# Kernel optimization log

Hardware: AMD Instinct MI355X
Metric: run time of the kernel (lower is better)

The kernel has to match this reference:

```python
import jax, jax.numpy as jnp
import numpy as np

N = 50000      # nodes
E = 800000     # edges (avg degree 16)
C = 5000       # clusters (Kongming compression)
D = 128        # in_features
OUT = 40       # out_features (classes)
K = 2          # propagation hops


def setup_inputs() -> dict:
    key = jax.random.key(0)
    k1, k2, k3, k4, k5, k6 = jax.random.split(key, 6)
    x = jax.random.normal(k1, (N, D), dtype=jnp.float32)
    edge_index = jax.random.randint(k2, (2, E), 0, N, dtype=jnp.int32)
    cluster_index = jax.random.randint(k3, (N,), 0, C, dtype=jnp.int32)
    rep_idx = jax.random.randint(k4, (C,), 0, N, dtype=jnp.int32)
    W = jax.random.normal(k5, (OUT, D), dtype=jnp.float32) / np.sqrt(D)
    b = jax.random.normal(k6, (OUT,), dtype=jnp.float32) * 0.01
    return {"x": x, "edge_index": edge_index, "cluster_index": cluster_index,
            "rep_idx": rep_idx, "W": W, "b": b}


def _gcn_propagate(x, edge_index, k_hops):
    # PUPropagate: K hops of D^{-1/2}(A+I)D^{-1/2} x (gcn_norm with self-loops)
    n = x.shape[0]
    loops = jnp.arange(n, dtype=edge_index.dtype)
    src = jnp.concatenate([edge_index[0], loops])
    dst = jnp.concatenate([edge_index[1], loops])
    deg = jax.ops.segment_sum(jnp.ones_like(src, dtype=x.dtype), dst, num_segments=n)
    dinv = jnp.where(deg > 0, jax.lax.rsqrt(deg), 0.0)
    norm = (dinv[src] * dinv[dst])[:, None]            # [E+N, 1]
    h = x
    for _ in range(k_hops):                            # small fixed hop count
        h = jax.ops.segment_sum(h[src] * norm, dst, num_segments=n)
    return h


def reference(x, edge_index, cluster_index, rep_idx, W, b):
    h = _gcn_propagate(x, edge_index, K)               # [N, D]
    # Kongming_Cluster: gather one representative row per cluster
    hc = h[rep_idx]                                    # [C, D]
    yc = hc @ W.T + b                                  # [C, OUT] dense linear on compressed rows
    # Kongming_Reconstruct: scatter back to all nodes by cluster index
    y = yc[cluster_index]                              # [N, OUT]
    return jax.nn.log_softmax(y, axis=1)
```

## Files before the change

### kernel.cpp

```cpp
#include <hip/hip_runtime.h>
#include <math.h>

#define N_NODES 50000
#define N_EDGES 800000
#define N_CLUST 5000
#define DIM     128
#define NOUT    40
#define SLOTS   64

#define FILL_PART   4
#define NODES_PER_P (N_NODES / FILL_PART)
#define FILL_CHUNKS 250
#define EI4         (N_EDGES / 4)
#define CI4         (EI4 / FILL_CHUNKS)

typedef __attribute__((ext_vector_type(8))) short short8;
typedef __attribute__((ext_vector_type(4))) float fvec4;
typedef __attribute__((ext_vector_type(4))) int ivec4;

__device__ __forceinline__ short bf16r(float v) {
    unsigned u = __float_as_uint(v);
    u = (u + 0x7FFFu + ((u >> 16) & 1u)) >> 16;
    return (short)u;
}
__device__ __forceinline__ unsigned pack_bf16x2(float a, float b) {
    unsigned ua = __float_as_uint(a);
    unsigned ub = __float_as_uint(b);
    ua = (ua + 0x7FFFu + ((ua >> 16) & 1u)) >> 16;
    ub = (ub + 0x7FFFu + ((ub >> 16) & 1u)) >> 16;
    return ua | (ub << 16);
}
__device__ __forceinline__ float2 unpack_bf16x2(unsigned v) {
    float2 r;
    r.x = __uint_as_float(v << 16);
    r.y = __uint_as_float(v & 0xFFFF0000u);
    return r;
}
__device__ __forceinline__ float4 unpack_bf16x4(uint2 v) {
    float4 r;
    r.x = __uint_as_float(v.x << 16);
    r.y = __uint_as_float(v.x & 0xFFFF0000u);
    r.z = __uint_as_float(v.y << 16);
    r.w = __uint_as_float(v.y & 0xFFFF0000u);
    return r;
}

__global__ __launch_bounds__(256) void fill_slots(const ivec4* __restrict__ src4,
                                                  const ivec4* __restrict__ dst4,
                                                  int* __restrict__ cnt,
                                                  unsigned short* __restrict__ slot) {
    int p = blockIdx.x & (FILL_PART - 1);
    int chunk = blockIdx.x >> 2;
    int lo = p * NODES_PER_P;
    int hi = lo + NODES_PER_P;
    int q0 = chunk * CI4;
    for (int i = threadIdx.x; i < CI4; i += 256) {
        ivec4 d4 = __builtin_nontemporal_load(&dst4[q0 + i]);
        ivec4 s4 = __builtin_nontemporal_load(&src4[q0 + i]);
        if (d4.x >= lo && d4.x < hi) {
            int pos = atomicAdd(&cnt[d4.x], 1);
            if (pos < SLOTS) slot[d4.x * SLOTS + pos] = (unsigned short)s4.x;
        }
        if (d4.y >= lo && d4.y < hi) {
            int pos = atomicAdd(&cnt[d4.y], 1);
            if (pos < SLOTS) slot[d4.y * SLOTS + pos] = (unsigned short)s4.y;
        }
        if (d4.z >= lo && d4.z < hi) {
            int pos = atomicAdd(&cnt[d4.z], 1);
            if (pos < SLOTS) slot[d4.z * SLOTS + pos] = (unsigned short)s4.z;
        }
        if (d4.w >= lo && d4.w < hi) {
            int pos = atomicAdd(&cnt[d4.w], 1);
            if (pos < SLOTS) slot[d4.w * SLOTS + pos] = (unsigned short)s4.w;
        }
    }
}

__global__ __launch_bounds__(256) void zgemm(const float* __restrict__ x,
                                             const float* __restrict__ W,
                                             const int* __restrict__ cnt,
                                             unsigned short* __restrict__ zs) {
    int lane = threadIdx.x & 63;
    int wv = threadIdx.x >> 6;
    int q = lane >> 4, r16 = lane & 15;
    int tile = blockIdx.x * 4 + wv;
    if (tile >= N_NODES / 16) return;

    short8 bfr[3][4];
    #pragma unroll
    for (int t = 0; t < 3; t++) {
        int o = t * 16 + r16;
        #pragma unroll
        for (int s = 0; s < 4; s++) {
            short8 f = {0, 0, 0, 0, 0, 0, 0, 0};
            if (o < NOUT) {
                const float* wp = W + o * DIM + s * 32 + q * 8;
                float4 w0 = *(const float4*)wp;
                float4 w1 = *(const float4*)(wp + 4);
                f[0] = bf16r(w0.x); f[1] = bf16r(w0.y);
                f[2] = bf16r(w0.z); f[3] = bf16r(w0.w);
                f[4] = bf16r(w1.x); f[5] = bf16r(w1.y);
                f[6] = bf16r(w1.z); f[7] = bf16r(w1.w);
            }
            bfr[t][s] = f;
        }
    }

    int node = tile * 16 + r16;
    float dn = rsqrtf((float)cnt[node] + 1.0f);
    short8 af[4];
    #pragma unroll
    for (int s = 0; s < 4; s++) {
        const float* xp = x + (size_t)node * DIM + s * 32 + q * 8;
        float4 a0 = *(const float4*)xp;
        float4 a1 = *(const float4*)(xp + 4);
        short8 f;
        f[0] = bf16r(dn * a0.x); f[1] = bf16r(dn * a0.y);
        f[2] = bf16r(dn * a0.z); f[3] = bf16r(dn * a0.w);
        f[4] = bf16r(dn * a1.x); f[5] = bf16r(dn * a1.y);
        f[6] = bf16r(dn * a1.z); f[7] = bf16r(dn * a1.w);
        af[s] = f;
    }

    fvec4 acc0 = {0, 0, 0, 0}, acc1 = {0, 0, 0, 0}, acc2 = {0, 0, 0, 0};
    #pragma unroll
    for (int s = 0; s < 4; s++) {
        acc0 = __builtin_amdgcn_mfma_f32_16x16x32_bf16(af[s], bfr[0][s], acc0, 0, 0, 0);
        acc1 = __builtin_amdgcn_mfma_f32_16x16x32_bf16(af[s], bfr[1][s], acc1, 0, 0, 0);
        acc2 = __builtin_amdgcn_mfma_f32_16x16x32_bf16(af[s], bfr[2][s], acc2, 0, 0, 0);
    }

    #pragma unroll
    for (int r = 0; r < 4; r++) {
        int nd = tile * 16 + q * 4 + r;
        unsigned short* zrow = zs + (size_t)nd * NOUT;
        zrow[r16]      = (unsigned short)bf16r(acc0[r]);
        zrow[16 + r16] = (unsigned short)bf16r(acc1[r]);
        if (r16 < 8) zrow[32 + r16] = (unsigned short)bf16r(acc2[r]);
    }
}

__global__ __launch_bounds__(256) void hop_all(const uint2* __restrict__ zs2,
                                               uint2* __restrict__ v12,
                                               const unsigned short* __restrict__ slot,
                                               const int* __restrict__ cnt) {
    int lane = threadIdx.x & 63;
    int g = lane / 10;
    int k = lane - g * 10;
    int wv = threadIdx.x >> 6;
    int n = blockIdx.x * 24 + wv * 6 + g;
    if (g >= 6 || n >= N_NODES) return;
    int c = cnt[n];
    int m = (c < SLOTS) ? c : SLOTS;
    float s = 1.0f / (float)(c + 1);
    float4 accA = unpack_bf16x4(zs2[n * 10 + k]);
    float4 accB; accB.x = accB.y = accB.z = accB.w = 0.0f;
    int base = n * SLOTS;
    int j = 0;
    for (; j + 7 < m; j += 8) {
        unsigned ss0 = *(const unsigned*)&slot[base + j];
        unsigned ss1 = *(const unsigned*)&slot[base + j + 2];
        unsigned ss2 = *(const unsigned*)&slot[base + j + 4];
        unsigned ss3 = *(const unsigned*)&slot[base + j + 6];
        float4 f0 = unpack_bf16x4(zs2[(int)(ss0 & 0xFFFFu) * 10 + k]);
        float4 f1 = unpack_bf16x4(zs2[(int)(ss0 >> 16) * 10 + k]);
        float4 f2 = unpack_bf16x4(zs2[(int)(ss1 & 0xFFFFu) * 10 + k]);
        float4 f3 = unpack_bf16x4(zs2[(int)(ss1 >> 16) * 10 + k]);
        float4 f4 = unpack_bf16x4(zs2[(int)(ss2 & 0xFFFFu) * 10 + k]);
        float4 f5 = unpack_bf16x4(zs2[(int)(ss2 >> 16) * 10 + k]);
        float4 f6 = unpack_bf16x4(zs2[(int)(ss3 & 0xFFFFu) * 10 + k]);
        float4 f7 = unpack_bf16x4(zs2[(int)(ss3 >> 16) * 10 + k]);
        accA.x += (f0.x + f1.x) + (f4.x + f5.x);
        accA.y += (f0.y + f1.y) + (f4.y + f5.y);
        accA.z += (f0.z + f1.z) + (f4.z + f5.z);
        accA.w += (f0.w + f1.w) + (f4.w + f5.w);
        accB.x += (f2.x + f3.x) + (f6.x + f7.x);
        accB.y += (f2.y + f3.y) + (f6.y + f7.y);
        accB.z += (f2.z + f3.z) + (f6.z + f7.z);
        accB.w += (f2.w + f3.w) + (f6.w + f7.w);
    }
    for (; j + 1 < m; j += 2) {
        unsigned ss0 = *(const unsigned*)&slot[base + j];
        float4 f0 = unpack_bf16x4(zs2[(int)(ss0 & 0xFFFFu) * 10 + k]);
        float4 f1 = unpack_bf16x4(zs2[(int)(ss0 >> 16) * 10 + k]);
        accA.x += f0.x + f1.x;  accA.y += f0.y + f1.y;
        accA.z += f0.z + f1.z;  accA.w += f0.w + f1.w;
    }
    if (j < m) {
        float4 f0 = unpack_bf16x4(zs2[(int)slot[base + j] * 10 + k]);
        accB.x += f0.x; accB.y += f0.y; accB.z += f0.z; accB.w += f0.w;
    }
    uint2 p;
    p.x = pack_bf16x2(s * (accA.x + accB.x), s * (accA.y + accB.y));
    p.y = pack_bf16x2(s * (accA.z + accB.z), s * (accA.w + accB.w));
    v12[n * 10 + k] = p;
}

__global__ __launch_bounds__(256) void rep_lsm(const unsigned* __restrict__ v1,
                                               const unsigned short* __restrict__ slot,
                                               const int* __restrict__ cnt,
                                               const int* __restrict__ rep_idx,
                                               const float2* __restrict__ b2,
                                               float2* __restrict__ yc2) {
    int lane = threadIdx.x & 63;
    int wv = threadIdx.x >> 6;
    int c = blockIdx.x * 4 + wv;
    if (c >= N_CLUST) return;
    int n = rep_idx[c];
    int cn = cnt[n];
    int m = (cn < SLOTS) ? cn : SLOTS;
    float dn = rsqrtf((float)(cn + 1));
    int g = lane / 20;
    int k = lane - g * 20;
    float2 acc; acc.x = 0.0f; acc.y = 0.0f;
    if (g == 0) acc = unpack_bf16x2(v1[n * 20 + k]);
    if (g < 3) {
        int base = n * SLOTS;
        for (int j = g; j < m; j += 3) {
            float2 f = unpack_bf16x2(v1[(int)slot[base + j] * 20 + k]);
            acc.x += f.x; acc.y += f.y;
        }
    }
    float t1x = __shfl(acc.x, lane + 20), t1y = __shfl(acc.y, lane + 20);
    float t2x = __shfl(acc.x, lane + 40), t2y = __shfl(acc.y, lane + 40);
    bool act = (lane < 20);
    float2 h; h.x = 0.0f; h.y = 0.0f;
    if (act) {
        float2 bb = b2[k];
        h.x = dn * (acc.x + t1x + t2x) + bb.x;
        h.y = dn * (acc.y + t1y + t2y) + bb.y;
    }
    float mx = act ? fmaxf(h.x, h.y) : -INFINITY;
    #pragma unroll
    for (int off = 32; off; off >>= 1) mx = fmaxf(mx, __shfl_xor(mx, off));
    float e = act ? (expf(h.x - mx) + expf(h.y - mx)) : 0.0f;
    #pragma unroll
    for (int off = 32; off; off >>= 1) e += __shfl_xor(e, off);
    float lg = mx + logf(e);
    if (act) {
        float2 o; o.x = h.x - lg; o.y = h.y - lg;
        yc2[(size_t)c * 20 + k] = o;
    }
}

__global__ void gather_out(const float4* __restrict__ yc4, const int* __restrict__ cidx,
                           float4* __restrict__ out4) {
    int t = blockIdx.x * blockDim.x + threadIdx.x;
    if (t >= N_NODES * (NOUT / 4)) return;
    int n = t / (NOUT / 4);
    int q = t - n * (NOUT / 4);
    out4[t] = yc4[(size_t)cidx[n] * (NOUT / 4) + q];
}

extern "C" void kernel_launch(void* const* d_in, const int* in_sizes, int n_in,
                              void* d_out, int out_size, void* d_ws, size_t ws_size,
                              hipStream_t stream) {
    const float* x    = (const float*)d_in[0];
    const int*   esrc = (const int*)d_in[1];
    const int*   edst = ((const int*)d_in[1]) + N_EDGES;
    const int*   cidx = (const int*)d_in[2];
    const int*   ridx = (const int*)d_in[3];
    const float* W    = (const float*)d_in[4];
    const float* b    = (const float*)d_in[5];
    float* out = (float*)d_out;

    char* ws = (char*)d_ws;
    size_t off = 0;
    auto alloc = [&](size_t bytes) { char* p = ws + off; off += (bytes + 255) & ~size_t(255); return p; };
    int*            cnt  = (int*)alloc(N_NODES * 4);
    unsigned short* slot = (unsigned short*)alloc((size_t)N_NODES * SLOTS * 2);
    unsigned short* zs   = (unsigned short*)alloc((size_t)N_NODES * NOUT * 2);
    unsigned*       v1   = (unsigned*)alloc((size_t)N_NODES * (NOUT / 2) * 4);
    float*          yc   = (float*)alloc((size_t)N_CLUST * NOUT * 4);
    (void)ws_size; (void)in_sizes; (void)n_in; (void)out_size;

    hipMemsetAsync(cnt, 0, N_NODES * 4, stream);

    const int B = 256;
    fill_slots<<<FILL_PART * FILL_CHUNKS, 256, 0, stream>>>((const ivec4*)esrc,
                                                            (const ivec4*)edst,
                                                            cnt, slot);
    zgemm<<<(N_NODES / 16 + 3) / 4, 256, 0, stream>>>(x, W, cnt, zs);
    hop_all<<<(N_NODES + 23) / 24, 256, 0, stream>>>((const uint2*)zs, (uint2*)v1,
                                                     slot, cnt);
    rep_lsm<<<(N_CLUST + 3) / 4, 256, 0, stream>>>((const unsigned*)v1, slot, cnt, ridx,
                                                   (const float2*)b, (float2*)yc);
    int gt = N_NODES * (NOUT / 4);
    gather_out<<<(gt + B - 1) / B, B, 0, stream>>>((const float4*)yc, cidx, (float4*)out);
}
```

Baseline: 162.3 us.

## Fuse slot fill, GEMM and cluster inversion; scatter log-softmax rows directly

The edge slot fill, the node GEMM and a new cluster-inverse build now run as disjoint block ranges of one launch, so the GEMM no longer waits for degrees. To make that possible, the degree normalisation moves out of the GEMM into the first hop, which now reads the degree of every neighbour. The cluster representative kernel writes its log-softmax row straight to every member node through the inverse lists, which drops the yc buffer and the gather kernel. In exchange the first hop does extra random degree reads, and clusters with more than 64 members would be silently truncated.

```diff
diff --git a/kernel.cpp b/kernel.cpp
--- a/kernel.cpp
+++ b/kernel.cpp
@@ -7,12 +7,18 @@
 #define DIM     128
 #define NOUT    40
 #define SLOTS   64
+#define CSLOT   64
 
 #define FILL_PART   4
 #define NODES_PER_P (N_NODES / FILL_PART)
 #define FILL_CHUNKS 250
 #define EI4         (N_EDGES / 4)
 #define CI4         (EI4 / FILL_CHUNKS)
+
+#define FILLB  1000
+#define ZB     782
+#define INVB   50
+#define GRID_A (FILLB + ZB + INVB)
 
 typedef __attribute__((ext_vector_type(8))) short short8;
 typedef __attribute__((ext_vector_type(4))) float fvec4;
@@ -45,98 +51,111 @@
     return r;
 }
 
-__global__ __launch_bounds__(256) void fill_slots(const ivec4* __restrict__ src4,
-                                                  const ivec4* __restrict__ dst4,
-                                                  int* __restrict__ cnt,
-                                                  unsigned short* __restrict__ slot) {
-    int p = blockIdx.x & (FILL_PART - 1);
-    int chunk = blockIdx.x >> 2;
-    int lo = p * NODES_PER_P;
-    int hi = lo + NODES_PER_P;
-    int q0 = chunk * CI4;
-    for (int i = threadIdx.x; i < CI4; i += 256) {
-        ivec4 d4 = __builtin_nontemporal_load(&dst4[q0 + i]);
-        ivec4 s4 = __builtin_nontemporal_load(&src4[q0 + i]);
-        if (d4.x >= lo && d4.x < hi) {
-            int pos = atomicAdd(&cnt[d4.x], 1);
-            if (pos < SLOTS) slot[d4.x * SLOTS + pos] = (unsigned short)s4.x;
-        }
-        if (d4.y >= lo && d4.y < hi) {
-            int pos = atomicAdd(&cnt[d4.y], 1);
-            if (pos < SLOTS) slot[d4.y * SLOTS + pos] = (unsigned short)s4.y;
-        }
-        if (d4.z >= lo && d4.z < hi) {
-            int pos = atomicAdd(&cnt[d4.z], 1);
-            if (pos < SLOTS) slot[d4.z * SLOTS + pos] = (unsigned short)s4.z;
-        }
-        if (d4.w >= lo && d4.w < hi) {
-            int pos = atomicAdd(&cnt[d4.w], 1);
-            if (pos < SLOTS) slot[d4.w * SLOTS + pos] = (unsigned short)s4.w;
-        }
-    }
-}
-
-__global__ __launch_bounds__(256) void zgemm(const float* __restrict__ x,
-                                             const float* __restrict__ W,
-                                             const int* __restrict__ cnt,
-                                             unsigned short* __restrict__ zs) {
+__global__ __launch_bounds__(256) void fused_A(const float* __restrict__ x,
+                                               const int* __restrict__ esrc,
+                                               const int* __restrict__ edst,
+                                               const int* __restrict__ cidx,
+                                               const float* __restrict__ W,
+                                               int* __restrict__ cnt,
+                                               int* __restrict__ ccnt,
+                                               unsigned short* __restrict__ slot,
+                                               unsigned short* __restrict__ zs,
+                                               unsigned short* __restrict__ cinv) {
     int lane = threadIdx.x & 63;
     int wv = threadIdx.x >> 6;
-    int q = lane >> 4, r16 = lane & 15;
-    int tile = blockIdx.x * 4 + wv;
-    if (tile >= N_NODES / 16) return;
-
-    short8 bfr[3][4];
-    #pragma unroll
-    for (int t = 0; t < 3; t++) {
-        int o = t * 16 + r16;
+
+    if (blockIdx.x < FILLB) {
+        const ivec4* src4 = (const ivec4*)esrc;
+        const ivec4* dst4 = (const ivec4*)edst;
+        int p = blockIdx.x & (FILL_PART - 1);
+        int chunk = blockIdx.x >> 2;
+        int lo = p * NODES_PER_P;
+        int hi = lo + NODES_PER_P;
+        int q0 = chunk * CI4;
+        for (int i = threadIdx.x; i < CI4; i += 256) {
+            ivec4 d4 = __builtin_nontemporal_load(&dst4[q0 + i]);
+            ivec4 s4 = __builtin_nontemporal_load(&src4[q0 + i]);
+            if (d4.x >= lo && d4.x < hi) {
+                int pos = atomicAdd(&cnt[d4.x], 1);
+                if (pos < SLOTS) slot[d4.x * SLOTS + pos] = (unsigned short)s4.x;
+            }
+            if (d4.y >= lo && d4.y < hi) {
+                int pos = atomicAdd(&cnt[d4.y], 1);
+                if (pos < SLOTS) slot[d4.y * SLOTS + pos] = (unsigned short)s4.y;
+            }
+            if (d4.z >= lo && d4.z < hi) {
+                int pos = atomicAdd(&cnt[d4.z], 1);
+                if (pos < SLOTS) slot[d4.z * SLOTS + pos] = (unsigned short)s4.z;
+            }
+            if (d4.w >= lo && d4.w < hi) {
+                int pos = atomicAdd(&cnt[d4.w], 1);
+                if (pos < SLOTS) slot[d4.w * SLOTS + pos] = (unsigned short)s4.w;
+            }
+        }
+    } else if (blockIdx.x < FILLB + ZB) {
+        int tile = (blockIdx.x - FILLB) * 4 + wv;
+        if (tile >= N_NODES / 16) return;
+        int q = lane >> 4, r16 = lane & 15;
+
+        short8 bfr[3][4];
+        #pragma unroll
+        for (int t = 0; t < 3; t++) {
+            int o = t * 16 + r16;
+            #pragma unroll
+            for (int s = 0; s < 4; s++) {
+                short8 f = {0, 0, 0, 0, 0, 0, 0, 0};
+                if (o < NOUT) {
+                    const float* wp = W + o * DIM + s * 32 + q * 8;
+                    float4 w0 = *(const float4*)wp;
+                    float4 w1 = *(const float4*)(wp + 4);
+                    f[0] = bf16r(w0.x); f[1] = bf16r(w0.y);
+                    f[2] = bf16r(w0.z); f[3] = bf16r(w0.w);
+                    f[4] = bf16r(w1.x); f[5] = bf16r(w1.y);
+                    f[6] = bf16r(w1.z); f[7] = bf16r(w1.w);
+                }
+                bfr[t][s] = f;
+            }
+        }
+
+        int node = tile * 16 + r16;
+        short8 af[4];
         #pragma unroll
         for (int s = 0; s < 4; s++) {
-            short8 f = {0, 0, 0, 0, 0, 0, 0, 0};
-            if (o < NOUT) {
-                const float* wp = W + o * DIM + s * 32 + q * 8;
-                float4 w0 = *(const float4*)wp;
-                float4 w1 = *(const float4*)(wp + 4);
-                f[0] = bf16r(w0.x); f[1] = bf16r(w0.y);
-                f[2] = bf16r(w0.z); f[3] = bf16r(w0.w);
-                f[4] = bf16r(w1.x); f[5] = bf16r(w1.y);
-                f[6] = bf16r(w1.z); f[7] = bf16r(w1.w);
-            }
-            bfr[t][s] = f;
-        }
-    }
-
-    int node = tile * 16 + r16;
-    float dn = rsqrtf((float)cnt[node] + 1.0f);
-    short8 af[4];
-    #pragma unroll
-    for (int s = 0; s < 4; s++) {
-        const float* xp = x + (size_t)node * DIM + s * 32 + q * 8;
-        float4 a0 = *(const float4*)xp;
-        float4 a1 = *(const float4*)(xp + 4);
-        short8 f;
-        f[0] = bf16r(dn * a0.x); f[1] = bf16r(dn * a0.y);
-        f[2] = bf16r(dn * a0.z); f[3] = bf16r(dn * a0.w);
-        f[4] = bf16r(dn * a1.x); f[5] = bf16r(dn * a1.y);
-        f[6] = bf16r(dn * a1.z); f[7] = bf16r(dn * a1.w);
-        af[s] = f;
-    }
-
-    fvec4 acc0 = {0, 0, 0, 0}, acc1 = {0, 0, 0, 0}, acc2 = {0, 0, 0, 0};
-    #pragma unroll
-    for (int s = 0; s < 4; s++) {
-        acc0 = __builtin_amdgcn_mfma_f32_16x16x32_bf16(af[s], bfr[0][s], acc0, 0, 0, 0);
-        acc1 = __builtin_amdgcn_mfma_f32_16x16x32_bf16(af[s], bfr[1][s], acc1, 0, 0, 0);
-        acc2 = __builtin_amdgcn_mfma_f32_16x16x32_bf16(af[s], bfr[2][s], acc2, 0, 0, 0);
-    }
-
-    #pragma unroll
-    for (int r = 0; r < 4; r++) {
-        int nd = tile * 16 + q * 4 + r;
-        unsigned short* zrow = zs + (size_t)nd * NOUT;
-        zrow[r16]      = (unsigned short)bf16r(acc0[r]);
-        zrow[16 + r16] = (unsigned short)bf16r(acc1[r]);
-        if (r16 < 8) zrow[32 + r16] = (unsigned short)bf16r(acc2[r]);
+            const fvec4* xp = (const fvec4*)(x + (size_t)node * DIM + s * 32 + q * 8);
+            fvec4 a0 = __builtin_nontemporal_load(xp);
+            fvec4 a1 = __builtin_nontemporal_load(xp + 1);
+            short8 f;
+            f[0] = bf16r(a0.x); f[1] = bf16r(a0.y);
+            f[2] = bf16r(a0.z); f[3] = bf16r(a0.w);
+            f[4] = bf16r(a1.x); f[5] = bf16r(a1.y);
+            f[6] = bf16r(a1.z); f[7] = bf16r(a1.w);
+            af[s] = f;
+        }
+
+        fvec4 acc0 = {0, 0, 0, 0}, acc1 = {0, 0, 0, 0}, acc2 = {0, 0, 0, 0};
+        #pragma unroll
+        for (int s = 0; s < 4; s++) {
+            acc0 = __builtin_amdgcn_mfma_f32_16x16x32_bf16(af[s], bfr[0][s], acc0, 0, 0, 0);
+            acc1 = __builtin_amdgcn_mfma_f32_16x16x32_bf16(af[s], bfr[1][s], acc1, 0, 0, 0);
+            acc2 = __builtin_amdgcn_mfma_f32_16x16x32_bf16(af[s], bfr[2][s], acc2, 0, 0, 0);
+        }
+
+        #pragma unroll
+        for (int r = 0; r < 4; r++) {
+            int nd = tile * 16 + q * 4 + r;
+            unsigned short* zrow = zs + (size_t)nd * NOUT;
+            __builtin_nontemporal_store((unsigned short)bf16r(acc0[r]), &zrow[r16]);
+            __builtin_nontemporal_store((unsigned short)bf16r(acc1[r]), &zrow[16 + r16]);
+            if (r16 < 8)
+                __builtin_nontemporal_store((unsigned short)bf16r(acc2[r]), &zrow[32 + r16]);
+        }
+    } else {
+        int t0 = (blockIdx.x - FILLB - ZB) * 256 + threadIdx.x;
+        for (int i = t0; i < N_NODES; i += INVB * 256) {
+            int c = cidx[i];
+            int pos = atomicAdd(&ccnt[c], 1);
+            if (pos < CSLOT) cinv[c * CSLOT + pos] = (unsigned short)i;
+        }
     }
 }
 
@@ -153,42 +172,38 @@
     int c = cnt[n];
     int m = (c < SLOTS) ? c : SLOTS;
     float s = 1.0f / (float)(c + 1);
-    float4 accA = unpack_bf16x4(zs2[n * 10 + k]);
+    float dn = rsqrtf((float)(c + 1));
+    float4 self = unpack_bf16x4(zs2[n * 10 + k]);
+    float4 accA;
+    accA.x = dn * self.x; accA.y = dn * self.y;
+    accA.z = dn * self.z; accA.w = dn * self.w;
     float4 accB; accB.x = accB.y = accB.z = accB.w = 0.0f;
     int base = n * SLOTS;
     int j = 0;
-    for (; j + 7 < m; j += 8) {
+    for (; j + 3 < m; j += 4) {
         unsigned ss0 = *(const unsigned*)&slot[base + j];
         unsigned ss1 = *(const unsigned*)&slot[base + j + 2];
-        unsigned ss2 = *(const unsigned*)&slot[base + j + 4];
-        unsigned ss3 = *(const unsigned*)&slot[base + j + 6];
-        float4 f0 = unpack_bf16x4(zs2[(int)(ss0 & 0xFFFFu) * 10 + k]);
-        float4 f1 = unpack_bf16x4(zs2[(int)(ss0 >> 16) * 10 + k]);
-        float4 f2 = unpack_bf16x4(zs2[(int)(ss1 & 0xFFFFu) * 10 + k]);
-        float4 f3 = unpack_bf16x4(zs2[(int)(ss1 >> 16) * 10 + k]);
-        float4 f4 = unpack_bf16x4(zs2[(int)(ss2 & 0xFFFFu) * 10 + k]);
-        float4 f5 = unpack_bf16x4(zs2[(int)(ss2 >> 16) * 10 + k]);
-        float4 f6 = unpack_bf16x4(zs2[(int)(ss3 & 0xFFFFu) * 10 + k]);
-        float4 f7 = unpack_bf16x4(zs2[(int)(ss3 >> 16) * 10 + k]);
-        accA.x += (f0.x + f1.x) + (f4.x + f5.x);
-        accA.y += (f0.y + f1.y) + (f4.y + f5.y);
-        accA.z += (f0.z + f1.z) + (f4.z + f5.z);
-        accA.w += (f0.w + f1.w) + (f4.w + f5.w);
-        accB.x += (f2.x + f3.x) + (f6.x + f7.x);
-        accB.y += (f2.y + f3.y) + (f6.y + f7.y);
-        accB.z += (f2.z + f3.z) + (f6.z + f7.z);
-        accB.w += (f2.w + f3.w) + (f6.w + f7.w);
-    }
-    for (; j + 1 < m; j += 2) {
-        unsigned ss0 = *(const unsigned*)&slot[base + j];
-        float4 f0 = unpack_bf16x4(zs2[(int)(ss0 & 0xFFFFu) * 10 + k]);
-        float4 f1 = unpack_bf16x4(zs2[(int)(ss0 >> 16) * 10 + k]);
-        accA.x += f0.x + f1.x;  accA.y += f0.y + f1.y;
-        accA.z += f0.z + f1.z;  accA.w += f0.w + f1.w;
-    }
-    if (j < m) {
-        float4 f0 = unpack_bf16x4(zs2[(int)slot[base + j] * 10 + k]);
-        accB.x += f0.x; accB.y += f0.y; accB.z += f0.z; accB.w += f0.w;
+        int s0 = (int)(ss0 & 0xFFFFu), s1 = (int)(ss0 >> 16);
+        int s2 = (int)(ss1 & 0xFFFFu), s3 = (int)(ss1 >> 16);
+        float d0 = rsqrtf((float)(cnt[s0] + 1));
+        float d1 = rsqrtf((float)(cnt[s1] + 1));
+        float d2 = rsqrtf((float)(cnt[s2] + 1));
+        float d3 = rsqrtf((float)(cnt[s3] + 1));
+        float4 f0 = unpack_bf16x4(zs2[s0 * 10 + k]);
+        float4 f1 = unpack_bf16x4(zs2[s1 * 10 + k]);
+        float4 f2 = unpack_bf16x4(zs2[s2 * 10 + k]);
+        float4 f3 = unpack_bf16x4(zs2[s3 * 10 + k]);
+        accA.x += d0 * f0.x + d1 * f1.x;  accA.y += d0 * f0.y + d1 * f1.y;
+        accA.z += d0 * f0.z + d1 * f1.z;  accA.w += d0 * f0.w + d1 * f1.w;
+        accB.x += d2 * f2.x + d3 * f3.x;  accB.y += d2 * f2.y + d3 * f3.y;
+        accB.z += d2 * f2.z + d3 * f3.z;  accB.w += d2 * f2.w + d3 * f3.w;
+    }
+    for (; j < m; j++) {
+        int s0 = (int)slot[base + j];
+        float d0 = rsqrtf((float)(cnt[s0] + 1));
+        float4 f0 = unpack_bf16x4(zs2[s0 * 10 + k]);
+        accB.x += d0 * f0.x; accB.y += d0 * f0.y;
+        accB.z += d0 * f0.z; accB.w += d0 * f0.w;
     }
     uint2 p;
     p.x = pack_bf16x2(s * (accA.x + accB.x), s * (accA.y + accB.y));
@@ -196,12 +211,14 @@
     v12[n * 10 + k] = p;
 }
 
-__global__ __launch_bounds__(256) void rep_lsm(const unsigned* __restrict__ v1,
-                                               const unsigned short* __restrict__ slot,
-                                               const int* __restrict__ cnt,
-                                               const int* __restrict__ rep_idx,
-                                               const float2* __restrict__ b2,
-                                               float2* __restrict__ yc2) {
+__global__ __launch_bounds__(256) void rep_scatter(const unsigned* __restrict__ v1,
+                                                   const unsigned short* __restrict__ slot,
+                                                   const int* __restrict__ cnt,
+                                                   const int* __restrict__ ccnt,
+                                                   const unsigned short* __restrict__ cinv,
+                                                   const int* __restrict__ rep_idx,
+                                                   const float2* __restrict__ b2,
+                                                   float2* __restrict__ out2) {
     int lane = threadIdx.x & 63;
     int wv = threadIdx.x >> 6;
     int c = blockIdx.x * 4 + wv;
@@ -237,19 +254,14 @@
     #pragma unroll
     for (int off = 32; off; off >>= 1) e += __shfl_xor(e, off);
     float lg = mx + logf(e);
-    if (act) {
-        float2 o; o.x = h.x - lg; o.y = h.y - lg;
-        yc2[(size_t)c * 20 + k] = o;
-    }
-}
-
-__global__ void gather_out(const float4* __restrict__ yc4, const int* __restrict__ cidx,
-                           float4* __restrict__ out4) {
-    int t = blockIdx.x * blockDim.x + threadIdx.x;
-    if (t >= N_NODES * (NOUT / 4)) return;
-    int n = t / (NOUT / 4);
-    int q = t - n * (NOUT / 4);
-    out4[t] = yc4[(size_t)cidx[n] * (NOUT / 4) + q];
+    float2 o; o.x = h.x - lg; o.y = h.y - lg;
+    int mc = ccnt[c];
+    if (mc > CSLOT) mc = CSLOT;
+    const unsigned short* mem = cinv + c * CSLOT;
+    for (int idx = 0; idx < mc; idx++) {
+        int node = (int)mem[idx];
+        if (act) out2[(size_t)node * 20 + k] = o;
+    }
 }
 
 extern "C" void kernel_launch(void* const* d_in, const int* in_sizes, int n_in,
@@ -267,24 +279,21 @@
     char* ws = (char*)d_ws;
     size_t off = 0;
     auto alloc = [&](size_t bytes) { char* p = ws + off; off += (bytes + 255) & ~size_t(255); return p; };
-    int*            cnt  = (int*)alloc(N_NODES * 4);
+    int*            cnt  = (int*)alloc((N_NODES + N_CLUST) * 4);
+    int*            ccnt = cnt + N_NODES;
     unsigned short* slot = (unsigned short*)alloc((size_t)N_NODES * SLOTS * 2);
     unsigned short* zs   = (unsigned short*)alloc((size_t)N_NODES * NOUT * 2);
     unsigned*       v1   = (unsigned*)alloc((size_t)N_NODES * (NOUT / 2) * 4);
-    float*          yc   = (float*)alloc((size_t)N_CLUST * NOUT * 4);
+    unsigned short* cinv = (unsigned short*)alloc((size_t)N_CLUST * CSLOT * 2);
     (void)ws_size; (void)in_sizes; (void)n_in; (void)out_size;
 
-    hipMemsetAsync(cnt, 0, N_NODES * 4, stream);
-
-    const int B = 256;
-    fill_slots<<<FILL_PART * FILL_CHUNKS, 256, 0, stream>>>((const ivec4*)esrc,
-                                                            (const ivec4*)edst,
-                                                            cnt, slot);
-    zgemm<<<(N_NODES / 16 + 3) / 4, 256, 0, stream>>>(x, W, cnt, zs);
+    hipMemsetAsync(cnt, 0, (N_NODES + N_CLUST) * 4, stream);
+
+    fused_A<<<GRID_A, 256, 0, stream>>>(x, esrc, edst, cidx, W,
+                                        cnt, ccnt, slot, zs, cinv);
     hop_all<<<(N_NODES + 23) / 24, 256, 0, stream>>>((const uint2*)zs, (uint2*)v1,
                                                      slot, cnt);
-    rep_lsm<<<(N_CLUST + 3) / 4, 256, 0, stream>>>((const unsigned*)v1, slot, cnt, ridx,
-                                                   (const float2*)b, (float2*)yc);
-    int gt = N_NODES * (NOUT / 4);
-    gather_out<<<(gt + B - 1) / B, B, 0, stream>>>((const float4*)yc, cidx, (float4*)out);
-}
+    rep_scatter<<<(N_CLUST + 3) / 4, 256, 0, stream>>>((const unsigned*)v1, slot, cnt,
+                                                       ccnt, cinv, ridx,
+                                                       (const float2*)b, (float2*)out);
+}
```

After: 161.6 us. No clear change (-0.4%).
